# Optimization experiments

Hardware: AMD Instinct MI355X
Metric: run time of the kernel (lower is better)

The kernel has to match this reference:

```python
import jax, jax.numpy as jnp
import numpy as np

DIM = 32
N_ENTITY = 500000
N_RELATION = 64
N_USER = 100000
N_ITEM = 200000
B = 4096
K = 64
L = 2


def setup_inputs() -> dict:
    key = jax.random.key(0)
    ks = jax.random.split(key, 14)
    users = jax.random.randint(ks[0], (B,), 0, N_USER)
    items = jax.random.randint(ks[1], (B,), 0, N_ITEM)
    hop0_items = jax.random.randint(ks[2], (B, K), 0, N_ENTITY)
    heads = jax.random.randint(ks[3], (L, B, K), 0, N_ENTITY)
    relations = jax.random.randint(ks[4], (L, B, K), 0, N_RELATION)
    tails = jax.random.randint(ks[5], (L, B, K), 0, N_ENTITY)
    # xavier-uniform-style embedding tables
    def xavier(k, shape):
        bound = float(np.sqrt(6.0 / (shape[0] + shape[1])))
        return jax.random.uniform(k, shape, jnp.float32, -bound, bound)
    entity_emb = xavier(ks[6], (N_ENTITY, DIM))
    relation_emb = xavier(ks[7], (N_RELATION, DIM))
    rec_user_emb = xavier(ks[8], (N_USER, DIM))
    rec_item_emb = xavier(ks[9], (N_ITEM, DIM))
    # RNN params (torch default init: U(-1/sqrt(hidden), 1/sqrt(hidden)))
    b = 1.0 / float(np.sqrt(DIM))
    W_ih = jax.random.uniform(ks[10], (DIM, 2 * DIM), jnp.float32, -b, b)
    W_hh = jax.random.uniform(ks[11], (DIM, DIM), jnp.float32, -b, b)
    b_ih = jax.random.uniform(ks[12], (DIM,), jnp.float32, -b, b)
    b_hh = jax.random.uniform(ks[13], (DIM,), jnp.float32, -b, b)
    return {
        "users": users, "items": items, "hop0_items": hop0_items,
        "heads": heads, "relations": relations, "tails": tails,
        "entity_emb": entity_emb, "relation_emb": relation_emb,
        "rec_user_emb": rec_user_emb, "rec_item_emb": rec_item_emb,
        "W_ih": W_ih, "W_hh": W_hh, "b_ih": b_ih, "b_hh": b_hh,
    }


def reference(users, items, hop0_items, heads, relations, tails,
              entity_emb, relation_emb, rec_user_emb, rec_item_emb,
              W_ih, W_hh, b_ih, b_hh):
    # hop-0: sum of item embeddings in each user's seed set  [B, dim]
    o = entity_emb[hop0_items].sum(axis=1)
    n_hops = heads.shape[0]
    for l in range(n_hops):
        h = entity_emb[heads[l]]        # [B, K, d]
        r = relation_emb[relations[l]]  # [B, K, d]
        tl = entity_emb[tails[l]]       # [B, K, d]
        hr = jnp.concatenate([h, r], axis=-1)   # [B, K, 2d]
        tr = jnp.concatenate([tl, r], axis=-1)  # [B, K, 2d]
        # attention over the K triples of each user
        pi = jax.nn.softmax((hr * tr).sum(axis=-1), axis=1)[..., None]  # [B,K,1]
        # 2-step tanh RNN over sequence (hr, tr), h0 = 0; take final hidden state
        h1 = jnp.tanh(jnp.einsum('bke,de->bkd', hr, W_ih) + b_ih + b_hh)
        h2 = jnp.tanh(jnp.einsum('bke,de->bkd', tr, W_ih)
                      + jnp.einsum('bkd,ed->bke', h1, W_hh) + b_ih + b_hh)
        o = o + (pi * h2).sum(axis=1)
    user_embeddings = o + rec_user_emb[users]
    item_embeddings = entity_emb[items] + rec_item_emb[items]
    return jax.nn.sigmoid((user_embeddings * item_embeddings).sum(axis=1))
```

## Files before the change

### kernel.cpp

```cpp
#include <hip/hip_runtime.h>

#define DIM 32
#define KK 64
#define WPB 4
#define WIH_STRIDE 144
#define WHH_STRIDE 80
#define H1_STRIDE 80
#define LDS_WIH (32 * WIH_STRIDE)
#define LDS_WHH (32 * WHH_STRIDE)
#define LDS_H1  (KK * H1_STRIDE)

typedef short bf16x8 __attribute__((ext_vector_type(8)));
typedef float f32x16 __attribute__((ext_vector_type(16)));
typedef unsigned int u32x4 __attribute__((ext_vector_type(4)));

__device__ __forceinline__ float rcp_fast(float x) { return __builtin_amdgcn_rcpf(x); }

__device__ __forceinline__ float tanh_fast(float x) {
    float t = __expf(2.0f * x);
    return 1.0f - 2.0f * rcp_fast(t + 1.0f);
}

__device__ __forceinline__ unsigned pk2(float lo, float hi) {
    return __builtin_amdgcn_perm(__builtin_bit_cast(unsigned, hi),
                                 __builtin_bit_cast(unsigned, lo), 0x07060302u);
}

__device__ __forceinline__ bf16x8 pack8(float4 a, float4 b) {
    u32x4 u;
    u[0] = pk2(a.x, a.y); u[1] = pk2(a.z, a.w);
    u[2] = pk2(b.x, b.y); u[3] = pk2(b.z, b.w);
    return __builtin_bit_cast(bf16x8, u);
}

__device__ __forceinline__ float dot4(float4 a, float4 b) {
    float s = a.x * b.x;
    s = fmaf(a.y, b.y, s); s = fmaf(a.z, b.z, s); s = fmaf(a.w, b.w, s);
    return s;
}

__global__ __launch_bounds__(256) void ripple_k1(
    const int* __restrict__ users,
    const int* __restrict__ items,
    const int* __restrict__ hop0_items,
    const int* __restrict__ heads,
    const int* __restrict__ relations,
    const int* __restrict__ tails,
    const float* __restrict__ entity_emb,
    const float* __restrict__ relation_emb,
    const float* __restrict__ rec_user_emb,
    const float* __restrict__ rec_item_emb,
    const float* __restrict__ W_ih,
    const float* __restrict__ W_hh,
    const float* __restrict__ b_ih,
    const float* __restrict__ b_hh,
    float* __restrict__ ws,
    const int B)
{
    __shared__ __align__(16) unsigned char lds[LDS_WIH + LDS_WHH + WPB * LDS_H1];
    unsigned char* wihL = lds;
    unsigned char* whhL = lds + LDS_WIH;
    unsigned char* h1L  = lds + LDS_WIH + LDS_WHH;

    const int tid = threadIdx.x;

    #pragma unroll
    for (int c = 0; c < 4; ++c) {
        int i = tid + 256 * c;
        int row = i >> 5, dw = i & 31;
        *(unsigned*)(wihL + row * WIH_STRIDE + dw * 4) =
            pk2(W_ih[row * 64 + 2 * dw], W_ih[row * 64 + 2 * dw + 1]);
    }
    #pragma unroll
    for (int c = 0; c < 2; ++c) {
        int i = tid + 256 * c;
        int row = i >> 4, dw = i & 15;
        *(unsigned*)(whhL + row * WHH_STRIDE + dw * 4) =
            pk2(W_hh[row * 32 + 2 * dw], W_hh[row * 32 + 2 * dw + 1]);
    }
    __syncthreads();

    const int wv   = tid >> 6;
    const int lane = tid & 63;
    const int h5   = lane >> 5;
    const int p    = lane & 31;
    const int w    = blockIdx.x * WPB + wv;
    if (w >= 3 * B) return;

    int role, b0;
    if (w < B)          { role = 0; b0 = w; }
    else if (w < 2 * B) { role = 1; b0 = w - B; }
    else                { role = 2; b0 = w - 2 * B; }
    const int b = __builtin_amdgcn_readfirstlane(b0);

    if (role == 0) {
        const int it = __builtin_amdgcn_readfirstlane(items[b]);
        const int uu = __builtin_amdgcn_readfirstlane(users[b]);
        float q[DIM];
        #pragma unroll
        for (int d = 0; d < DIM; ++d)
            q[d] = entity_emb[(size_t)it * DIM + d] + rec_item_emb[(size_t)it * DIM + d];
        float up = 0.0f;
        #pragma unroll
        for (int d = 0; d < DIM; ++d)
            up = fmaf(rec_user_emb[(size_t)uu * DIM + d], q[d], up);

        const int idx = hop0_items[b * KK + lane];
        const float4* rp = (const float4*)(entity_emb + (size_t)idx * DIM);
        float part = 0.0f;
        #pragma unroll
        for (int i = 0; i < 8; ++i) {
            float4 v = rp[i];
            part = fmaf(v.x, q[4*i+0], part);
            part = fmaf(v.y, q[4*i+1], part);
            part = fmaf(v.z, q[4*i+2], part);
            part = fmaf(v.w, q[4*i+3], part);
        }
        #pragma unroll
        for (int m = 1; m <= 32; m <<= 1) part += __shfl_xor(part, m, 64);
        if (lane == 0) ws[b] = part + up;
        return;
    }

    const int l = role - 1;
    const int base = (l * B + b) * KK;

    const int iAh = heads[base + p],       iBh = heads[base + 32 + p];
    const int iAr = relations[base + p],   iBr = relations[base + 32 + p];
    const int iAt = tails[base + p],       iBt = tails[base + 32 + p];

    float4 gh[8], gt[8], gr[8];
    {
        const float* a = entity_emb + (size_t)iAh * DIM + 8 * h5;
        const float* bb_ = entity_emb + (size_t)iBh * DIM + 8 * h5;
        gh[0] = *(const float4*)(a);      gh[1] = *(const float4*)(a + 4);
        gh[2] = *(const float4*)(a + 16); gh[3] = *(const float4*)(a + 20);
        gh[4] = *(const float4*)(bb_);      gh[5] = *(const float4*)(bb_ + 4);
        gh[6] = *(const float4*)(bb_ + 16); gh[7] = *(const float4*)(bb_ + 20);
    }
    {
        const float* a = entity_emb + (size_t)iAt * DIM + 8 * h5;
        const float* bb_ = entity_emb + (size_t)iBt * DIM + 8 * h5;
        gt[0] = *(const float4*)(a);      gt[1] = *(const float4*)(a + 4);
        gt[2] = *(const float4*)(a + 16); gt[3] = *(const float4*)(a + 20);
        gt[4] = *(const float4*)(bb_);      gt[5] = *(const float4*)(bb_ + 4);
        gt[6] = *(const float4*)(bb_ + 16); gt[7] = *(const float4*)(bb_ + 20);
    }
    {
        const float* a = relation_emb + (size_t)iAr * DIM + 8 * h5;
        const float* bb_ = relation_emb + (size_t)iBr * DIM + 8 * h5;
        gr[0] = *(const float4*)(a);      gr[1] = *(const float4*)(a + 4);
        gr[2] = *(const float4*)(a + 16); gr[3] = *(const float4*)(a + 20);
        gr[4] = *(const float4*)(bb_);      gr[5] = *(const float4*)(bb_ + 4);
        gr[6] = *(const float4*)(bb_ + 16); gr[7] = *(const float4*)(bb_ + 20);
    }

    const int it = __builtin_amdgcn_readfirstlane(items[b]);
    float qf[16], bv[16];
    #pragma unroll
    for (int Q = 0; Q < 4; ++Q) {
        const int d0 = 8 * Q + 4 * h5;
        float4 qe = *(const float4*)(entity_emb   + (size_t)it * DIM + d0);
        float4 qr = *(const float4*)(rec_item_emb + (size_t)it * DIM + d0);
        float4 bi = *(const float4*)(b_ih + d0);
        float4 bh = *(const float4*)(b_hh + d0);
        qf[4*Q+0] = qe.x + qr.x; qf[4*Q+1] = qe.y + qr.y;
        qf[4*Q+2] = qe.z + qr.z; qf[4*Q+3] = qe.w + qr.w;
        bv[4*Q+0] = bi.x + bh.x; bv[4*Q+1] = bi.y + bh.y;
        bv[4*Q+2] = bi.z + bh.z; bv[4*Q+3] = bi.w + bh.w;
    }

    float scA = 0.0f, scB = 0.0f;
    #pragma unroll
    for (int i = 0; i < 4; ++i) {
        scA += dot4(gh[i], gt[i]);
        scA += dot4(gr[i], gr[i]);
    }
    #pragma unroll
    for (int i = 4; i < 8; ++i) {
        scB += dot4(gh[i], gt[i]);
        scB += dot4(gr[i], gr[i]);
    }

    bf16x8 hf[2][2], tf[2][2], rf[2][2];
    #pragma unroll
    for (int nt = 0; nt < 2; ++nt)
        #pragma unroll
        for (int kt = 0; kt < 2; ++kt) {
            hf[nt][kt] = pack8(gh[nt*4 + kt*2], gh[nt*4 + kt*2 + 1]);
            tf[nt][kt] = pack8(gt[nt*4 + kt*2], gt[nt*4 + kt*2 + 1]);
            rf[nt][kt] = pack8(gr[nt*4 + kt*2], gr[nt*4 + kt*2 + 1]);
        }

    bf16x8 wihF[4], whhF[2];
    #pragma unroll
    for (int kt = 0; kt < 4; ++kt)
        wihF[kt] = __builtin_bit_cast(bf16x8,
            *(const u32x4*)(wihL + p * WIH_STRIDE + kt * 32 + h5 * 16));
    #pragma unroll
    for (int kt = 0; kt < 2; ++kt)
        whhF[kt] = __builtin_bit_cast(bf16x8,
            *(const u32x4*)(whhL + p * WHH_STRIDE + kt * 32 + h5 * 16));

    f32x16 accA[2], accB[2];
    {
        f32x16 bias_v;
        #pragma unroll
        for (int j = 0; j < 16; ++j) bias_v[j] = bv[j];
        accA[0] = bias_v; accA[1] = bias_v;
    }
    #pragma unroll
    for (int nt = 0; nt < 2; ++nt)
        #pragma unroll
        for (int kt = 0; kt < 2; ++kt)
            accA[nt] = __builtin_amdgcn_mfma_f32_32x32x16_bf16(
                wihF[2 + kt], rf[nt][kt], accA[nt], 0, 0, 0);
    accB[0] = accA[0]; accB[1] = accA[1];
    #pragma unroll
    for (int nt = 0; nt < 2; ++nt)
        #pragma unroll
        for (int kt = 0; kt < 2; ++kt)
            accB[nt] = __builtin_amdgcn_mfma_f32_32x32x16_bf16(
                wihF[kt], hf[nt][kt], accB[nt], 0, 0, 0);
    #pragma unroll
    for (int nt = 0; nt < 2; ++nt)
        #pragma unroll
        for (int kt = 0; kt < 2; ++kt)
            accA[nt] = __builtin_amdgcn_mfma_f32_32x32x16_bf16(
                wihF[kt], tf[nt][kt], accA[nt], 0, 0, 0);

    unsigned char* myh1 = h1L + wv * LDS_H1;
    #pragma unroll
    for (int nt = 0; nt < 2; ++nt) {
        float t0[16];
        #pragma unroll
        for (int j = 0; j < 16; ++j) t0[j] = tanh_fast(accB[nt][j]);
        unsigned char* hrow = myh1 + (32 * nt + p) * H1_STRIDE;
        #pragma unroll
        for (int Q = 0; Q < 4; ++Q) {
            uint2 wq;
            wq.x = pk2(t0[4*Q+0], t0[4*Q+1]);
            wq.y = pk2(t0[4*Q+2], t0[4*Q+3]);
            *(uint2*)(hrow + 16 * Q + 8 * h5) = wq;
        }
    }
    #pragma unroll
    for (int nt = 0; nt < 2; ++nt)
        #pragma unroll
        for (int kt = 0; kt < 2; ++kt) {
            bf16x8 h1f = __builtin_bit_cast(bf16x8,
                *(const u32x4*)(myh1 + (32 * nt + p) * H1_STRIDE + (2 * kt + h5) * 16));
            accA[nt] = __builtin_amdgcn_mfma_f32_32x32x16_bf16(
                whhF[kt], h1f, accA[nt], 0, 0, 0);
        }

    scA += __shfl_xor(scA, 32, 64);
    scB += __shfl_xor(scB, 32, 64);
    const float e0 = __expf(scA);
    const float e1 = __expf(scB);

    float sd0 = 0.0f, sd1 = 0.0f;
    #pragma unroll
    for (int j = 0; j < 16; ++j) sd0 = fmaf(tanh_fast(accA[0][j]), qf[j], sd0);
    #pragma unroll
    for (int j = 0; j < 16; ++j) sd1 = fmaf(tanh_fast(accA[1][j]), qf[j], sd1);
    sd0 += __shfl_xor(sd0, 32, 64);
    sd1 += __shfl_xor(sd1, 32, 64);

    float num = e0 * sd0 + e1 * sd1;
    float den = e0 + e1;
    #pragma unroll
    for (int m = 1; m <= 16; m <<= 1) {
        num += __shfl_xor(num, m, 64);
        den += __shfl_xor(den, m, 64);
    }
    if (lane == 0) ws[(1 + l) * B + b] = num * rcp_fast(den);
}

__global__ __launch_bounds__(256) void ripple_k2(
    const float* __restrict__ ws, float* __restrict__ out, const int B)
{
    const int i = blockIdx.x * 256 + threadIdx.x;
    if (i < B) {
        const float s = ws[i] + ws[B + i] + ws[2 * B + i];
        out[i] = rcp_fast(1.0f + __expf(-s));
    }
}

extern "C" void kernel_launch(void* const* d_in, const int* in_sizes, int n_in,
                              void* d_out, int out_size, void* d_ws, size_t ws_size,
                              hipStream_t stream)
{
    const int* users = (const int*)d_in[0];
    const int* items = (const int*)d_in[1];
    const int* hop0  = (const int*)d_in[2];
    const int* heads = (const int*)d_in[3];
    const int* rels  = (const int*)d_in[4];
    const int* tails = (const int*)d_in[5];
    const float* entity_emb   = (const float*)d_in[6];
    const float* relation_emb = (const float*)d_in[7];
    const float* rec_user_emb = (const float*)d_in[8];
    const float* rec_item_emb = (const float*)d_in[9];
    const float* W_ih = (const float*)d_in[10];
    const float* W_hh = (const float*)d_in[11];
    const float* b_ih = (const float*)d_in[12];
    const float* b_hh = (const float*)d_in[13];
    float* out = (float*)d_out;
    float* ws  = (float*)d_ws;

    const int B = in_sizes[0];
    const int blocks1 = (3 * B + WPB - 1) / WPB;
    hipLaunchKernelGGL(ripple_k1, dim3(blocks1), dim3(256), 0, stream,
                       users, items, hop0, heads, rels, tails,
                       entity_emb, relation_emb, rec_user_emb, rec_item_emb,
                       W_ih, W_hh, b_ih, b_hh, ws, B);
    const int blocks2 = (B + 255) / 256;
    hipLaunchKernelGGL(ripple_k2, dim3(blocks2), dim3(256), 0, stream,
                       ws, out, B);
}
```

Baseline: 49.84 us.

## Replace LDS h1 staging with cross-lane shuffles and restructure hop-0 gather

The per-wave LDS buffer that held the first RNN hidden state is removed. The bf16 MFMA operand is now built in registers with xor-32 lane shuffles, which cuts LDS use and adds a launch-bounds hint requesting 3 blocks per CU. The hop-0 role now gathers each seed row with two half-waves and vectorized loads, matching the hop-role layout, and the item/bias vectors are loaded uniformly then selected per half. The shuffles add cross-lane traffic and the uniform 32-element loads may raise register pressure.

Measured after the change: 54.32 us. +9.0%, slower.

```diff
diff --git a/kernel.cpp b/kernel.cpp
--- a/kernel.cpp
+++ b/kernel.cpp
@@ -5,10 +5,8 @@
 #define WPB 4
 #define WIH_STRIDE 144
 #define WHH_STRIDE 80
-#define H1_STRIDE 80
 #define LDS_WIH (32 * WIH_STRIDE)
 #define LDS_WHH (32 * WHH_STRIDE)
-#define LDS_H1  (KK * H1_STRIDE)
 
 typedef short bf16x8 __attribute__((ext_vector_type(8)));
 typedef float f32x16 __attribute__((ext_vector_type(16)));
@@ -39,7 +37,7 @@
     return s;
 }
 
-__global__ __launch_bounds__(256) void ripple_k1(
+__global__ __launch_bounds__(256, 3) void ripple_k1(
     const int* __restrict__ users,
     const int* __restrict__ items,
     const int* __restrict__ hop0_items,
@@ -57,10 +55,9 @@
     float* __restrict__ ws,
     const int B)
 {
-    __shared__ __align__(16) unsigned char lds[LDS_WIH + LDS_WHH + WPB * LDS_H1];
+    __shared__ __align__(16) unsigned char lds[LDS_WIH + LDS_WHH];
     unsigned char* wihL = lds;
     unsigned char* whhL = lds + LDS_WIH;
-    unsigned char* h1L  = lds + LDS_WIH + LDS_WHH;
 
     const int tid = threadIdx.x;
 
@@ -96,6 +93,19 @@
     if (role == 0) {
         const int it = __builtin_amdgcn_readfirstlane(items[b]);
         const int uu = __builtin_amdgcn_readfirstlane(users[b]);
+        const int iA = hop0_items[b * KK + p];
+        const int iB = hop0_items[b * KK + 32 + p];
+        const float* a0 = entity_emb + (size_t)iA * DIM + 8 * h5;
+        const float* b0p = entity_emb + (size_t)iB * DIM + 8 * h5;
+        float4 vA0 = *(const float4*)(a0);
+        float4 vA1 = *(const float4*)(a0 + 4);
+        float4 vA2 = *(const float4*)(a0 + 16);
+        float4 vA3 = *(const float4*)(a0 + 20);
+        float4 vB0 = *(const float4*)(b0p);
+        float4 vB1 = *(const float4*)(b0p + 4);
+        float4 vB2 = *(const float4*)(b0p + 16);
+        float4 vB3 = *(const float4*)(b0p + 20);
+
         float q[DIM];
         #pragma unroll
         for (int d = 0; d < DIM; ++d)
@@ -105,17 +115,21 @@
         for (int d = 0; d < DIM; ++d)
             up = fmaf(rec_user_emb[(size_t)uu * DIM + d], q[d], up);
 
-        const int idx = hop0_items[b * KK + lane];
-        const float4* rp = (const float4*)(entity_emb + (size_t)idx * DIM);
-        float part = 0.0f;
-        #pragma unroll
-        for (int i = 0; i < 8; ++i) {
-            float4 v = rp[i];
-            part = fmaf(v.x, q[4*i+0], part);
-            part = fmaf(v.y, q[4*i+1], part);
-            part = fmaf(v.z, q[4*i+2], part);
-            part = fmaf(v.w, q[4*i+3], part);
-        }
+        float4 c0a, c0b, c1a, c1b;
+        {
+            float tmp[16];
+            #pragma unroll
+            for (int e = 0; e < 8; ++e) {
+                tmp[e]     = h5 ? q[8 + e]  : q[e];
+                tmp[8 + e] = h5 ? q[24 + e] : q[16 + e];
+            }
+            c0a = make_float4(tmp[0], tmp[1], tmp[2], tmp[3]);
+            c0b = make_float4(tmp[4], tmp[5], tmp[6], tmp[7]);
+            c1a = make_float4(tmp[8], tmp[9], tmp[10], tmp[11]);
+            c1b = make_float4(tmp[12], tmp[13], tmp[14], tmp[15]);
+        }
+        float part = dot4(vA0, c0a) + dot4(vA1, c0b) + dot4(vA2, c1a) + dot4(vA3, c1b)
+                   + dot4(vB0, c0a) + dot4(vB1, c0b) + dot4(vB2, c1a) + dot4(vB3, c1b);
         #pragma unroll
         for (int m = 1; m <= 32; m <<= 1) part += __shfl_xor(part, m, 64);
         if (lane == 0) ws[b] = part + up;
@@ -132,43 +146,44 @@
     float4 gh[8], gt[8], gr[8];
     {
         const float* a = entity_emb + (size_t)iAh * DIM + 8 * h5;
-        const float* bb_ = entity_emb + (size_t)iBh * DIM + 8 * h5;
+        const float* c = entity_emb + (size_t)iBh * DIM + 8 * h5;
         gh[0] = *(const float4*)(a);      gh[1] = *(const float4*)(a + 4);
         gh[2] = *(const float4*)(a + 16); gh[3] = *(const float4*)(a + 20);
-        gh[4] = *(const float4*)(bb_);      gh[5] = *(const float4*)(bb_ + 4);
-        gh[6] = *(const float4*)(bb_ + 16); gh[7] = *(const float4*)(bb_ + 20);
+        gh[4] = *(const float4*)(c);      gh[5] = *(const float4*)(c + 4);
+        gh[6] = *(const float4*)(c + 16); gh[7] = *(const float4*)(c + 20);
     }
     {
         const float* a = entity_emb + (size_t)iAt * DIM + 8 * h5;
-        const float* bb_ = entity_emb + (size_t)iBt * DIM + 8 * h5;
+        const float* c = entity_emb + (size_t)iBt * DIM + 8 * h5;
         gt[0] = *(const float4*)(a);      gt[1] = *(const float4*)(a + 4);
         gt[2] = *(const float4*)(a + 16); gt[3] = *(const float4*)(a + 20);
-        gt[4] = *(const float4*)(bb_);      gt[5] = *(const float4*)(bb_ + 4);
-        gt[6] = *(const float4*)(bb_ + 16); gt[7] = *(const float4*)(bb_ + 20);
+        gt[4] = *(const float4*)(c);      gt[5] = *(const float4*)(c + 4);
+        gt[6] = *(const float4*)(c + 16); gt[7] = *(const float4*)(c + 20);
     }
     {
         const float* a = relation_emb + (size_t)iAr * DIM + 8 * h5;
-        const float* bb_ = relation_emb + (size_t)iBr * DIM + 8 * h5;
+        const float* c = relation_emb + (size_t)iBr * DIM + 8 * h5;
         gr[0] = *(const float4*)(a);      gr[1] = *(const float4*)(a + 4);
         gr[2] = *(const float4*)(a + 16); gr[3] = *(const float4*)(a + 20);
-        gr[4] = *(const float4*)(bb_);      gr[5] = *(const float4*)(bb_ + 4);
-        gr[6] = *(const float4*)(bb_ + 16); gr[7] = *(const float4*)(bb_ + 20);
+        gr[4] = *(const float4*)(c);      gr[5] = *(const float4*)(c + 4);
+        gr[6] = *(const float4*)(c + 16); gr[7] = *(const float4*)(c + 20);
     }
 
     const int it = __builtin_amdgcn_readfirstlane(items[b]);
+    float qu[DIM], bu[DIM];
+    #pragma unroll
+    for (int d = 0; d < DIM; ++d) {
+        qu[d] = entity_emb[(size_t)it * DIM + d] + rec_item_emb[(size_t)it * DIM + d];
+        bu[d] = b_ih[d] + b_hh[d];
+    }
     float qf[16], bv[16];
     #pragma unroll
-    for (int Q = 0; Q < 4; ++Q) {
-        const int d0 = 8 * Q + 4 * h5;
-        float4 qe = *(const float4*)(entity_emb   + (size_t)it * DIM + d0);
-        float4 qr = *(const float4*)(rec_item_emb + (size_t)it * DIM + d0);
-        float4 bi = *(const float4*)(b_ih + d0);
-        float4 bh = *(const float4*)(b_hh + d0);
-        qf[4*Q+0] = qe.x + qr.x; qf[4*Q+1] = qe.y + qr.y;
-        qf[4*Q+2] = qe.z + qr.z; qf[4*Q+3] = qe.w + qr.w;
-        bv[4*Q+0] = bi.x + bh.x; bv[4*Q+1] = bi.y + bh.y;
-        bv[4*Q+2] = bi.z + bh.z; bv[4*Q+3] = bi.w + bh.w;
-    }
+    for (int Q = 0; Q < 4; ++Q)
+        #pragma unroll
+        for (int j = 0; j < 4; ++j) {
+            qf[4*Q+j] = h5 ? qu[8*Q + 4 + j] : qu[8*Q + j];
+            bv[4*Q+j] = h5 ? bu[8*Q + 4 + j] : bu[8*Q + j];
+        }
 
     float scA = 0.0f, scB = 0.0f;
     #pragma unroll
@@ -229,29 +244,31 @@
             accA[nt] = __builtin_amdgcn_mfma_f32_32x32x16_bf16(
                 wihF[kt], tf[nt][kt], accA[nt], 0, 0, 0);
 
-    unsigned char* myh1 = h1L + wv * LDS_H1;
-    #pragma unroll
-    for (int nt = 0; nt < 2; ++nt) {
-        float t0[16];
-        #pragma unroll
-        for (int j = 0; j < 16; ++j) t0[j] = tanh_fast(accB[nt][j]);
-        unsigned char* hrow = myh1 + (32 * nt + p) * H1_STRIDE;
+    unsigned dwA[2][4], dwB[2][4];
+    #pragma unroll
+    for (int nt = 0; nt < 2; ++nt)
         #pragma unroll
         for (int Q = 0; Q < 4; ++Q) {
-            uint2 wq;
-            wq.x = pk2(t0[4*Q+0], t0[4*Q+1]);
-            wq.y = pk2(t0[4*Q+2], t0[4*Q+3]);
-            *(uint2*)(hrow + 16 * Q + 8 * h5) = wq;
-        }
-    }
+            dwA[nt][Q] = pk2(tanh_fast(accB[nt][4*Q+0]), tanh_fast(accB[nt][4*Q+1]));
+            dwB[nt][Q] = pk2(tanh_fast(accB[nt][4*Q+2]), tanh_fast(accB[nt][4*Q+3]));
+        }
     #pragma unroll
     for (int nt = 0; nt < 2; ++nt)
         #pragma unroll
         for (int kt = 0; kt < 2; ++kt) {
-            bf16x8 h1f = __builtin_bit_cast(bf16x8,
-                *(const u32x4*)(myh1 + (32 * nt + p) * H1_STRIDE + (2 * kt + h5) * 16));
+            const unsigned ownA = h5 ? dwA[nt][2*kt+1] : dwA[nt][2*kt];
+            const unsigned ownB = h5 ? dwB[nt][2*kt+1] : dwB[nt][2*kt];
+            const unsigned sndA = h5 ? dwA[nt][2*kt]   : dwA[nt][2*kt+1];
+            const unsigned sndB = h5 ? dwB[nt][2*kt]   : dwB[nt][2*kt+1];
+            const unsigned rcvA = __shfl_xor(sndA, 32, 64);
+            const unsigned rcvB = __shfl_xor(sndB, 32, 64);
+            u32x4 u;
+            u[0] = h5 ? rcvA : ownA;
+            u[1] = h5 ? rcvB : ownB;
+            u[2] = h5 ? ownA : rcvA;
+            u[3] = h5 ? ownB : rcvB;
             accA[nt] = __builtin_amdgcn_mfma_f32_32x32x16_bf16(
-                whhF[kt], h1f, accA[nt], 0, 0, 0);
+                whhF[kt], __builtin_bit_cast(bf16x8, u), accA[nt], 0, 0, 0);
         }
 
     scA += __shfl_xor(scA, 32, 64);
```
